# Performance work log

Measured on AMD Instinct MI355X. Metric: run time of the kernel, lower is better.

Reference implementation:

```python
import jax, jax.numpy as jnp
import numpy as np

IN, H, OUT = 8, 256, 24  # input_size, hidden_size, output_size
B, T = 2048, 256


def _gate_step(hx, x, Wx, Wh, b):
    # Fused version of the 8 per-gate Linears: one [.,IN]@[IN,4H] + one [.,H]@[H,4H]
    gates = x @ Wx + hx @ Wh + b            # [B, 4H]
    i, f, o, g = jnp.split(gates, 4, axis=-1)
    i, f, o = jax.nn.sigmoid(i), jax.nn.sigmoid(f), jax.nn.sigmoid(o)
    g = jnp.tanh(g)
    # NOTE: in the original code cx is never reassigned, so it stays zeros and
    # cy = cx*f + i*g == i*g on every step. We replicate that exactly.
    cy = i * g
    return o * jnp.tanh(cy)


def setup_inputs() -> dict:
    key = jax.random.key(0)
    ks = jax.random.split(key, 9)
    s = 0.05
    return {
        "inputs0": jax.random.normal(ks[0], (B, T, IN), jnp.float32),
        "inputs1": jax.random.normal(ks[1], (B, OUT - 1), jnp.float32),
        # concatenated gate weights, order [i | f | o | c]
        "Wx": jax.random.normal(ks[2], (IN, 4 * H), jnp.float32) * s,
        "Wh": jax.random.normal(ks[3], (H, 4 * H), jnp.float32) * s,
        "b": jax.random.normal(ks[4], (4 * H,), jnp.float32) * s,  # bx + bh folded
        "Wy": jax.random.normal(ks[5], (H, 1), jnp.float32) * s,
        "by": jax.random.normal(ks[6], (1,), jnp.float32) * s,
        # fresh random Linear(1, IN) per decoder step in the original -> per-step params
        "dec_w": jax.random.normal(ks[7], (OUT - 1, IN), jnp.float32) * s,
        "dec_b": jax.random.normal(ks[8], (OUT - 1, IN), jnp.float32) * s,
    }


def reference(inputs0, inputs1, Wx, Wh, b, Wy, by, dec_w, dec_b):
    bsz = inputs0.shape[0]
    h0 = jnp.zeros((bsz, H), inputs0.dtype)

    # ---- encoder: scan over time (strict recurrence) ----
    x_seq = jnp.transpose(inputs0, (1, 0, 2))  # [T, B, IN]

    def enc_step(h, x):
        return _gate_step(h, x, Wx, Wh, b), None

    h, _ = jax.lax.scan(enc_step, h0, x_seq)
    hy0 = h @ Wy + by                           # [B, 1]

    # ---- decoder: OUT-1 steps, each with its own fresh 1->IN linear ----
    x1_seq = jnp.transpose(inputs1, (1, 0))[: OUT - 1]  # [OUT-1, B]

    def dec_step(h, inp):
        x1, w, bb = inp
        x = x1[:, None] * w[None, :] + bb[None, :]      # [B, IN]
        h = _gate_step(h, x, Wx, Wh, b)
        return h, h @ Wy + by                            # y: [B, 1]

    _, ys = jax.lax.scan(dec_step, h, (x1_seq, dec_w, dec_b))  # ys: [OUT-1, B, 1]

    hy = jnp.concatenate([hy0, jnp.transpose(ys[..., 0], (1, 0))], axis=1)  # [B, OUT]
    return hy
```

## Files before the change

### kernel.cpp

```cpp
#include <hip/hip_runtime.h>


typedef short bf16x8 __attribute__((ext_vector_type(8)));
typedef float f32x4 __attribute__((ext_vector_type(4)));

#define T_ENC 256
#define N_DEC 23
#define NSTEP 279
#define PV_T 28
#define PA_T 8
#define LDS_T 18
#define AFRAG 2304

__device__ __forceinline__ short f2bf(float f) {
  unsigned u = __float_as_uint(f);
  u = (u + 0x7fffu + ((u >> 16) & 1u)) >> 16;
  return (short)u;
}
__device__ __forceinline__ float bf2f(short s) {
  return __uint_as_float(((unsigned)(unsigned short)s) << 16);
}

#if __has_builtin(__builtin_amdgcn_rcpf)
#define RCPF(x) __builtin_amdgcn_rcpf(x)
#else
#define RCPF(x) (1.0f / (x))
#endif
#if __has_builtin(__builtin_amdgcn_exp2f)
#define EXP2(x) __builtin_amdgcn_exp2f(x)
#else
#define EXP2(x) __exp2f(x)
#endif

__global__ void pack_kernel(const float* __restrict__ Wx, const float* __restrict__ Wh,
                            const float* __restrict__ b, short* __restrict__ Wpack) {
  int tau = blockIdx.x;
  int l = threadIdx.x;
  int n_tile = tau / 9, kt = tau % 9;
  int w = n_tile / 6, t = n_tile % 6;
  int gate = t >> 1, loc = t & 1;
  int base = (gate == 0) ? 0 : (gate == 1 ? 512 : 768);
  float scale = (gate == 2) ? 2.885390082f : 1.442695041f;
  int c = l & 15, q = l >> 4;
  int oc = base + w * 32 + loc * 16 + c;
  bf16x8 v;
#pragma unroll
  for (int e = 0; e < 8; ++e) {
    int k = kt * 32 + q * 8 + e;
    float f;
    if (k < 256)       f = Wh[k * 1024 + oc];
    else if (k < 264)  f = Wx[(k - 256) * 1024 + oc];
    else if (k == 264) f = b[oc];
    else               f = 0.0f;
    v[e] = f2bf(f * scale);
  }
  ((bf16x8*)Wpack)[tau * 64 + l] = v;
}

__global__ __launch_bounds__(512, 2) void lstm_kernel(
    const float* __restrict__ inputs0, const float* __restrict__ inputs1,
    const float* __restrict__ Wy, const float* __restrict__ by,
    const float* __restrict__ dec_w, const float* __restrict__ dec_b,
    const short* __restrict__ Wpack, float* __restrict__ out) {
  __shared__ __align__(16) short B_lds[8 * LDS_T * 512];
  __shared__ __align__(16) short A_lds[2][AFRAG];
  __shared__ float Wy_lds[256];
  __shared__ float ypart[128];

  const int tid = threadIdx.x;
  const int wg = blockIdx.x;
  const int lane = tid & 63;
  const int w = tid >> 6;
  const int q = lane >> 4;
  const int c = lane & 15;

  const bf16x8* wp = (const bf16x8*)Wpack;

  bf16x8 Bv[PV_T];
#pragma unroll
  for (int r = 0; r < PV_T; ++r) {
    bf16x8 t0 = wp[(w * 54 + r) * 64 + lane];
    asm("" : "=v"(Bv[r]) : "0"(t0));
  }
  bf16x8 Ba[PA_T];
#pragma unroll
  for (int r = 0; r < PA_T; ++r) {
    bf16x8 t0 = wp[(w * 54 + PV_T + r) * 64 + lane];
    asm("" : "=a"(Ba[r]) : "0"(t0));
  }
#pragma unroll
  for (int j = 0; j < LDS_T; ++j) {
    bf16x8 v = wp[(w * 54 + PV_T + PA_T + j) * 64 + lane];
    *(bf16x8*)(B_lds + (w * LDS_T + j) * 512 + lane * 8) = v;
  }

  for (int i = tid; i < 2 * AFRAG; i += 512) A_lds[0][i] = 0;
  if (tid < 256) Wy_lds[tid] = Wy[tid];
  __syncthreads();

  if (tid < 64)
    A_lds[0][2048 + tid] = f2bf(inputs0[((wg * 8 + (tid >> 3)) * 256 + 0) * 8 + (tid & 7)]);
  if (tid < 16)
    A_lds[tid >> 3][2112 + (tid & 7) * 8] = (short)0x3F80;
  const float byv = by[0];
  __syncthreads();

#define LDSB(j) (*(const bf16x8*)(B_lds + (w * LDS_T + (j)) * 512 + lane * 8))

  const int qh = q >> 1;
  const int row0 = (q & 1) * 4;
  const int woff = w * 256 + (qh * 2 + (c >> 3)) * 64 + row0 * 8 + (c & 7);
  const int abase = q * 64 + (c & 7) * 8;

  f32x4 z4;
  z4[0] = 0.f; z4[1] = 0.f; z4[2] = 0.f; z4[3] = 0.f;
  asm("" : "+v"(z4));

  for (int s = 0; s < NSTEP; ++s) {
    const short* Ab = &A_lds[s & 1][0];
    short* An = &A_lds[(s + 1) & 1][0];

    float xv = 0.0f;
    const bool do_x = (tid < 64) && (s + 1 < NSTEP);
    if (do_x) {
      int sn = s + 1, xm = tid >> 3, xk = tid & 7;
      if (sn < T_ENC) {
        xv = inputs0[((wg * 8 + xm) * 256 + sn) * 8 + xk];
      } else {
        int d = sn - T_ENC;
        xv = inputs1[(wg * 8 + xm) * N_DEC + d] * dec_w[d * 8 + xk] + dec_b[d * 8 + xk];
      }
    }

    bf16x8 A[9];
#pragma unroll
    for (int kt = 0; kt < 9; ++kt)
      A[kt] = *(const bf16x8*)(Ab + kt * 256 + abase);

    __builtin_amdgcn_s_setprio(1);
    f32x4 a0 = __builtin_amdgcn_mfma_f32_16x16x32_bf16(A[0], Bv[0], z4, 0, 0, 0);
    f32x4 a1 = __builtin_amdgcn_mfma_f32_16x16x32_bf16(A[0], Bv[9], z4, 0, 0, 0);
#pragma unroll
    for (int kt = 1; kt < 9; ++kt) {
      a0 = __builtin_amdgcn_mfma_f32_16x16x32_bf16(A[kt], Bv[kt], a0, 0, 0, 0);
      a1 = __builtin_amdgcn_mfma_f32_16x16x32_bf16(A[kt], Bv[9 + kt], a1, 0, 0, 0);
    }
    __builtin_amdgcn_s_setprio(0);
    float ii[4];
    {
      const f32x4 vi = qh ? a1 : a0;
#pragma unroll
      for (int j = 0; j < 4; ++j) ii[j] = RCPF(1.0f + EXP2(-vi[j]));
    }

    __builtin_amdgcn_s_setprio(1);
    a0 = __builtin_amdgcn_mfma_f32_16x16x32_bf16(A[0], Bv[18], z4, 0, 0, 0);
    a1 = __builtin_amdgcn_mfma_f32_16x16x32_bf16(A[0], Bv[27], z4, 0, 0, 0);
#pragma unroll
    for (int kt = 1; kt < 9; ++kt) {
      a0 = __builtin_amdgcn_mfma_f32_16x16x32_bf16(A[kt], Bv[18 + kt], a0, 0, 0, 0);
      a1 = __builtin_amdgcn_mfma_f32_16x16x32_bf16(A[kt], Ba[kt - 1], a1, 0, 0, 0);
    }
    __builtin_amdgcn_s_setprio(0);
    float oo[4];
    {
      const f32x4 vo = qh ? a1 : a0;
#pragma unroll
      for (int j = 0; j < 4; ++j) oo[j] = RCPF(1.0f + EXP2(-vo[j]));
    }

    __builtin_amdgcn_s_setprio(1);
    a0 = __builtin_amdgcn_mfma_f32_16x16x32_bf16(A[0], LDSB(0), z4, 0, 0, 0);
    a1 = __builtin_amdgcn_mfma_f32_16x16x32_bf16(A[0], LDSB(9), z4, 0, 0, 0);
#pragma unroll
    for (int kt = 1; kt < 9; ++kt) {
      a0 = __builtin_amdgcn_mfma_f32_16x16x32_bf16(A[kt], LDSB(kt), a0, 0, 0, 0);
      a1 = __builtin_amdgcn_mfma_f32_16x16x32_bf16(A[kt], LDSB(9 + kt), a1, 0, 0, 0);
    }
    __builtin_amdgcn_s_setprio(0);
    {
      const f32x4 vg = qh ? a1 : a0;
      unsigned pk01, pk23;
      float hh[4];
#pragma unroll
      for (int j = 0; j < 4; ++j) {
        float gg = 1.0f - 2.0f * RCPF(EXP2(vg[j]) + 1.0f);
        float cy = ii[j] * gg;
        float t2 = 1.0f - 2.0f * RCPF(EXP2(cy * 2.885390082f) + 1.0f);
        hh[j] = oo[j] * t2;
      }
      asm("v_cvt_pk_bf16_f32 %0, %1, %2" : "=v"(pk01) : "v"(hh[0]), "v"(hh[1]));
      asm("v_cvt_pk_bf16_f32 %0, %1, %2" : "=v"(pk23) : "v"(hh[2]), "v"(hh[3]));
      An[woff + 0 * 8] = (short)(pk01 & 0xffffu);
      An[woff + 1 * 8] = (short)(pk01 >> 16);
      An[woff + 2 * 8] = (short)(pk23 & 0xffffu);
      An[woff + 3 * 8] = (short)(pk23 >> 16);
    }
    if (do_x) An[2048 + tid] = f2bf(xv);
    __syncthreads();

    if (s >= T_ENC - 1) {
      if (tid < 128) {
        int m = tid & 7, kq = tid >> 3;
        const short* hp = An + (kq >> 1) * 256 + (kq & 1) * 128 + m * 8;
        bf16x8 h0 = *(const bf16x8*)(hp);
        bf16x8 h1 = *(const bf16x8*)(hp + 64);
        float part = 0.0f;
#pragma unroll
        for (int j = 0; j < 8; ++j) {
          part += bf2f(h0[j]) * Wy_lds[kq * 16 + j];
          part += bf2f(h1[j]) * Wy_lds[kq * 16 + 8 + j];
        }
        ypart[tid] = part;
      }
      __syncthreads();
      if (tid < 8) {
        float y = byv;
#pragma unroll
        for (int kq = 0; kq < 16; ++kq) y += ypart[kq * 8 + tid];
        out[(wg * 8 + tid) * 24 + (s - (T_ENC - 1))] = y;
      }
      __syncthreads();
    }
  }
}

extern "C" void kernel_launch(void* const* d_in, const int* in_sizes, int n_in,
                              void* d_out, int out_size, void* d_ws, size_t ws_size,
                              hipStream_t stream) {
  const float* inputs0 = (const float*)d_in[0];
  const float* inputs1 = (const float*)d_in[1];
  const float* Wx      = (const float*)d_in[2];
  const float* Wh      = (const float*)d_in[3];
  const float* b       = (const float*)d_in[4];
  const float* Wy      = (const float*)d_in[5];
  const float* by      = (const float*)d_in[6];
  const float* dec_w   = (const float*)d_in[7];
  const float* dec_b   = (const float*)d_in[8];

  short* Wpack = (short*)d_ws;

  pack_kernel<<<dim3(432), dim3(64), 0, stream>>>(Wx, Wh, b, Wpack);
  lstm_kernel<<<dim3(256), dim3(512), 0, stream>>>(
      inputs0, inputs1, Wy, by, dec_w, dec_b, Wpack, (float*)d_out);
}
```

Measured before the change: 424.4 us.

## Defer output projection into next step, drop extra barriers, reorder gate matmuls

Result: no change. 429.0 us (+1.1%).

```diff
diff --git a/kernel.cpp b/kernel.cpp
--- a/kernel.cpp
+++ b/kernel.cpp
@@ -40,7 +40,7 @@
   int w = n_tile / 6, t = n_tile % 6;
   int gate = t >> 1, loc = t & 1;
   int base = (gate == 0) ? 0 : (gate == 1 ? 512 : 768);
-  float scale = (gate == 2) ? 2.885390082f : 1.442695041f;
+  float scale = (gate == 2) ? 2.885390082f : -1.442695041f;
   int c = l & 15, q = l >> 4;
   int oc = base + w * 32 + loc * 16 + c;
   bf16x8 v;
@@ -65,7 +65,6 @@
   __shared__ __align__(16) short B_lds[8 * LDS_T * 512];
   __shared__ __align__(16) short A_lds[2][AFRAG];
   __shared__ float Wy_lds[256];
-  __shared__ float ypart[128];
 
   const int tid = threadIdx.x;
   const int wg = blockIdx.x;
@@ -120,10 +119,28 @@
     const short* Ab = &A_lds[s & 1][0];
     short* An = &A_lds[(s + 1) & 1][0];
 
+    if (w == 0 && s >= 256) {
+      int m = lane >> 3, c8 = lane & 7;
+      const short* hp = Ab + c8 * 256 + m * 8;
+      float part = 0.0f;
+#pragma unroll
+      for (int qq = 0; qq < 4; ++qq) {
+        bf16x8 hv = *(const bf16x8*)(hp + qq * 64);
+#pragma unroll
+        for (int e = 0; e < 8; ++e)
+          part += bf2f(hv[e]) * Wy_lds[c8 * 32 + qq * 8 + e];
+      }
+      part += __shfl_xor(part, 1);
+      part += __shfl_xor(part, 2);
+      part += __shfl_xor(part, 4);
+      if (c8 == 0) out[(wg * 8 + m) * 24 + (s - 256)] = part + byv;
+    }
+
     float xv = 0.0f;
-    const bool do_x = (tid < 64) && (s + 1 < NSTEP);
+    const bool do_x = (tid >= 448) && (s + 1 < NSTEP);
+    const int xl = tid - 448;
     if (do_x) {
-      int sn = s + 1, xm = tid >> 3, xk = tid & 7;
+      int sn = s + 1, xm = xl >> 3, xk = xl & 7;
       if (sn < T_ENC) {
         xv = inputs0[((wg * 8 + xm) * 256 + sn) * 8 + xk];
       } else {
@@ -150,7 +167,27 @@
     {
       const f32x4 vi = qh ? a1 : a0;
 #pragma unroll
-      for (int j = 0; j < 4; ++j) ii[j] = RCPF(1.0f + EXP2(-vi[j]));
+      for (int j = 0; j < 4; ++j) ii[j] = RCPF(1.0f + EXP2(vi[j]));
+    }
+
+    __builtin_amdgcn_s_setprio(1);
+    a0 = __builtin_amdgcn_mfma_f32_16x16x32_bf16(A[0], LDSB(0), z4, 0, 0, 0);
+    a1 = __builtin_amdgcn_mfma_f32_16x16x32_bf16(A[0], LDSB(9), z4, 0, 0, 0);
+#pragma unroll
+    for (int kt = 1; kt < 9; ++kt) {
+      a0 = __builtin_amdgcn_mfma_f32_16x16x32_bf16(A[kt], LDSB(kt), a0, 0, 0, 0);
+      a1 = __builtin_amdgcn_mfma_f32_16x16x32_bf16(A[kt], LDSB(9 + kt), a1, 0, 0, 0);
+    }
+    __builtin_amdgcn_s_setprio(0);
+    float t2[4];
+    {
+      const f32x4 vg = qh ? a1 : a0;
+#pragma unroll
+      for (int j = 0; j < 4; ++j) {
+        float gg = 1.0f - 2.0f * RCPF(EXP2(vg[j]) + 1.0f);
+        float cy = ii[j] * gg;
+        t2[j] = 1.0f - 2.0f * RCPF(EXP2(cy * 2.885390082f) + 1.0f);
+      }
     }
 
     __builtin_amdgcn_s_setprio(1);
@@ -162,33 +199,13 @@
       a1 = __builtin_amdgcn_mfma_f32_16x16x32_bf16(A[kt], Ba[kt - 1], a1, 0, 0, 0);
     }
     __builtin_amdgcn_s_setprio(0);
-    float oo[4];
     {
       const f32x4 vo = qh ? a1 : a0;
-#pragma unroll
-      for (int j = 0; j < 4; ++j) oo[j] = RCPF(1.0f + EXP2(-vo[j]));
-    }
-
-    __builtin_amdgcn_s_setprio(1);
-    a0 = __builtin_amdgcn_mfma_f32_16x16x32_bf16(A[0], LDSB(0), z4, 0, 0, 0);
-    a1 = __builtin_amdgcn_mfma_f32_16x16x32_bf16(A[0], LDSB(9), z4, 0, 0, 0);
-#pragma unroll
-    for (int kt = 1; kt < 9; ++kt) {
-      a0 = __builtin_amdgcn_mfma_f32_16x16x32_bf16(A[kt], LDSB(kt), a0, 0, 0, 0);
-      a1 = __builtin_amdgcn_mfma_f32_16x16x32_bf16(A[kt], LDSB(9 + kt), a1, 0, 0, 0);
-    }
-    __builtin_amdgcn_s_setprio(0);
-    {
-      const f32x4 vg = qh ? a1 : a0;
+      float hh[4];
+#pragma unroll
+      for (int j = 0; j < 4; ++j)
+        hh[j] = RCPF(1.0f + EXP2(vo[j])) * t2[j];
       unsigned pk01, pk23;
-      float hh[4];
-#pragma unroll
-      for (int j = 0; j < 4; ++j) {
-        float gg = 1.0f - 2.0f * RCPF(EXP2(vg[j]) + 1.0f);
-        float cy = ii[j] * gg;
-        float t2 = 1.0f - 2.0f * RCPF(EXP2(cy * 2.885390082f) + 1.0f);
-        hh[j] = oo[j] * t2;
-      }
       asm("v_cvt_pk_bf16_f32 %0, %1, %2" : "=v"(pk01) : "v"(hh[0]), "v"(hh[1]));
       asm("v_cvt_pk_bf16_f32 %0, %1, %2" : "=v"(pk23) : "v"(hh[2]), "v"(hh[3]));
       An[woff + 0 * 8] = (short)(pk01 & 0xffffu);
@@ -196,32 +213,26 @@
       An[woff + 2 * 8] = (short)(pk23 & 0xffffu);
       An[woff + 3 * 8] = (short)(pk23 >> 16);
     }
-    if (do_x) An[2048 + tid] = f2bf(xv);
+    if (do_x) An[2048 + xl] = f2bf(xv);
     __syncthreads();
-
-    if (s >= T_ENC - 1) {
-      if (tid < 128) {
-        int m = tid & 7, kq = tid >> 3;
-        const short* hp = An + (kq >> 1) * 256 + (kq & 1) * 128 + m * 8;
-        bf16x8 h0 = *(const bf16x8*)(hp);
-        bf16x8 h1 = *(const bf16x8*)(hp + 64);
-        float part = 0.0f;
-#pragma unroll
-        for (int j = 0; j < 8; ++j) {
-          part += bf2f(h0[j]) * Wy_lds[kq * 16 + j];
-          part += bf2f(h1[j]) * Wy_lds[kq * 16 + 8 + j];
-        }
-        ypart[tid] = part;
-      }
-      __syncthreads();
-      if (tid < 8) {
-        float y = byv;
-#pragma unroll
-        for (int kq = 0; kq < 16; ++kq) y += ypart[kq * 8 + tid];
-        out[(wg * 8 + tid) * 24 + (s - (T_ENC - 1))] = y;
-      }
-      __syncthreads();
-    }
+  }
+
+  if (w == 0) {
+    const short* Ab = &A_lds[NSTEP & 1][0];
+    int m = lane >> 3, c8 = lane & 7;
+    const short* hp = Ab + c8 * 256 + m * 8;
+    float part = 0.0f;
+#pragma unroll
+    for (int qq = 0; qq < 4; ++qq) {
+      bf16x8 hv = *(const bf16x8*)(hp + qq * 64);
+#pragma unroll
+      for (int e = 0; e < 8; ++e)
+        part += bf2f(hv[e]) * Wy_lds[c8 * 32 + qq * 8 + e];
+    }
+    part += __shfl_xor(part, 1);
+    part += __shfl_xor(part, 2);
+    part += __shfl_xor(part, 4);
+    if (c8 == 0) out[(wg * 8 + m) * 24 + 23] = part + byv;
   }
 }
 
```
